# Kernel optimization log

Hardware: AMD Instinct MI355X
Metric: run time of the kernel (lower is better)

Reference implementation:

```python
import jax, jax.numpy as jnp
import numpy as np

ENC_DIM, DEC_DIM, ATT_DIM = 512, 512, 256
B, T = 64, 4096


def setup_inputs() -> dict:
    key = jax.random.key(0)
    ks = jax.random.split(key, 7)
    s_enc = 1.0 / np.sqrt(ENC_DIM)
    s_dec = 1.0 / np.sqrt(DEC_DIM)
    s_att = 1.0 / np.sqrt(ATT_DIM)
    return {
        "encoder_features": jax.random.normal(ks[0], (B, T, ENC_DIM), jnp.float32),
        "decoder_hidden": jax.random.normal(ks[1], (B, DEC_DIM), jnp.float32),
        # encoder_proj: Linear(encoder_dim, attention_dim) with bias
        "W_enc": jax.random.uniform(ks[2], (ENC_DIM, ATT_DIM), jnp.float32, -s_enc, s_enc),
        "b_enc": jax.random.uniform(ks[3], (ATT_DIM,), jnp.float32, -s_enc, s_enc),
        # decoder_proj: Linear(decoder_dim, attention_dim, bias=False)
        "W_dec": jax.random.uniform(ks[4], (DEC_DIM, ATT_DIM), jnp.float32, -s_dec, s_dec),
        # attention_vector: Linear(attention_dim, 1) with bias
        "v_att": jax.random.uniform(ks[5], (ATT_DIM,), jnp.float32, -s_att, s_att),
        "b_att": jax.random.uniform(ks[6], (), jnp.float32, -s_att, s_att),
    }


def reference(encoder_features, decoder_hidden, W_enc, b_enc, W_dec, v_att, b_att):
    # (B,T,A) = (B,T,E)@(E,A) + b
    enc_proj = jnp.einsum("bte,ea->bta", encoder_features, W_enc) + b_enc
    # (B,1,A)
    dec_proj = (decoder_hidden @ W_dec)[:, None, :]
    energy = jnp.tanh(enc_proj + dec_proj)                      # (B,T,A)
    scores = jnp.einsum("bta,a->bt", energy, v_att) + b_att     # (B,T)
    attention_weights = jax.nn.softmax(scores, axis=1)          # (B,T)
    context = jnp.einsum("bt,bte->be", attention_weights, encoder_features)
    return (context, attention_weights)
```

## Files before the change

kernel.cpp:

```cpp
#include <hip/hip_runtime.h>
#include <hip/hip_bf16.h>

#define E_DIM 512
#define D_DIM 512
#define A_DIM 256
#define B_SZ  64
#define T_SZ  4096
#define TT    64
#define NTB   (T_SZ / TT)
#define LDT   (E_DIM + 8)

typedef __bf16 bf16_t;
typedef bf16_t bf16x8 __attribute__((ext_vector_type(8)));
typedef float  f32x4  __attribute__((ext_vector_type(4)));

__device__ __forceinline__ unsigned short f2bf(float x) {
    union { float f; unsigned int u; } v; v.f = x;
    unsigned int u = v.u;
    return (unsigned short)((u + 0x7FFFu + ((u >> 16) & 1u)) >> 16);
}
__device__ __forceinline__ float bf_lo(unsigned int pk) {
    union { unsigned int u; float f; } v; v.u = pk << 16; return v.f;
}
__device__ __forceinline__ float bf_hi(unsigned int pk) {
    union { unsigned int u; float f; } v; v.u = pk & 0xFFFF0000u; return v.f;
}
__device__ __forceinline__ float tanh_fast(float x) {
    x = fminf(8.0f, fmaxf(-8.0f, x));
    float e = __expf(2.0f * x);
    return 1.0f - 2.0f * __builtin_amdgcn_rcpf(e + 1.0f);
}

__global__ __launch_bounds__(256) void prep_kernel(
    const float* __restrict__ dec, const float* __restrict__ W_enc,
    const float* __restrict__ b_enc, const float* __restrict__ W_dec,
    float* __restrict__ dp, unsigned short* __restrict__ Wt)
{
    const int bid = blockIdx.x, tid = threadIdx.x;
    if (bid < B_SZ) {
        float s = b_enc[tid];
        const float* dr = dec + bid * D_DIM;
        #pragma unroll 8
        for (int d = 0; d < D_DIM; ++d)
            s = fmaf(dr[d], W_dec[d * A_DIM + tid], s);
        dp[bid * A_DIM + tid] = s;
    } else {
        int base = (bid - B_SZ) * 2048;
        #pragma unroll
        for (int i = 0; i < 8; ++i) {
            int idx = base + tid + i * 256;
            int a = idx >> 9, e = idx & 511;
            Wt[idx] = f2bf(W_enc[e * A_DIM + a]);
        }
    }
}

__global__ __launch_bounds__(256, 2) void attn_main(
    const float* __restrict__ enc, const unsigned short* __restrict__ Wt,
    const float* __restrict__ dpg, const float* __restrict__ vatt,
    float* __restrict__ u_out, float* __restrict__ ctx_part)
{
    const int tb = blockIdx.x, b = blockIdx.y;
    const int tid = threadIdx.x;
    __shared__ unsigned short tile[TT * LDT];
    __shared__ float spart[4][TT];
    __shared__ float uu[TT];
    __shared__ float dp_s[A_DIM];
    __shared__ float vv[A_DIM];

    dp_s[tid] = dpg[b * A_DIM + tid];
    vv[tid]   = vatt[tid];

    const float4* src = (const float4*)(enc + ((size_t)b * T_SZ + (size_t)tb * TT) * E_DIM);
    #pragma unroll 4
    for (int it = 0; it < 32; ++it) {
        int idx = tid + it * 256;
        int r = idx >> 7, c = idx & 127;
        float4 v4 = src[idx];
        ushort4 h;
        h.x = f2bf(v4.x); h.y = f2bf(v4.y); h.z = f2bf(v4.z); h.w = f2bf(v4.w);
        *(ushort4*)&tile[r * LDT + c * 4] = h;
    }
    __syncthreads();

    const int w = tid >> 6, lane = tid & 63;
    const int m16 = lane & 15, q = lane >> 4;
    f32x4 acc[4][4];
    #pragma unroll
    for (int mi = 0; mi < 4; ++mi)
        #pragma unroll
        for (int ni = 0; ni < 4; ++ni)
            acc[mi][ni] = (f32x4){0.f, 0.f, 0.f, 0.f};

    for (int k0 = 0; k0 < E_DIM; k0 += 32) {
        const int ka = k0 + q * 8;
        bf16x8 afr[4], bfr[4];
        #pragma unroll
        for (int mi = 0; mi < 4; ++mi)
            afr[mi] = *(const bf16x8*)&tile[(mi * 16 + m16) * LDT + ka];
        #pragma unroll
        for (int ni = 0; ni < 4; ++ni)
            bfr[ni] = *(const bf16x8*)&Wt[(w * 64 + ni * 16 + m16) * E_DIM + ka];
        #pragma unroll
        for (int mi = 0; mi < 4; ++mi)
            #pragma unroll
            for (int ni = 0; ni < 4; ++ni)
                acc[mi][ni] = __builtin_amdgcn_mfma_f32_16x16x32_bf16(
                    afr[mi], bfr[ni], acc[mi][ni], 0, 0, 0);
    }

    float va[4], dpv[4];
    #pragma unroll
    for (int ni = 0; ni < 4; ++ni) {
        int a = w * 64 + ni * 16 + m16;
        va[ni] = vv[a]; dpv[ni] = dp_s[a];
    }
    #pragma unroll
    for (int mi = 0; mi < 4; ++mi) {
        #pragma unroll
        for (int r = 0; r < 4; ++r) {
            float p = 0.f;
            #pragma unroll
            for (int ni = 0; ni < 4; ++ni)
                p += va[ni] * tanh_fast(acc[mi][ni][r] + dpv[ni]);
            p += __shfl_xor(p, 1); p += __shfl_xor(p, 2);
            p += __shfl_xor(p, 4); p += __shfl_xor(p, 8);
            if (m16 == 0) spart[w][mi * 16 + q * 4 + r] = p;
        }
    }
    __syncthreads();

    if (tid < TT) {
        float s = spart[0][tid] + spart[1][tid] + spart[2][tid] + spart[3][tid];
        float e = __expf(s);
        uu[tid] = e;
        u_out[(size_t)b * T_SZ + (size_t)tb * TT + tid] = e;
    }
    __syncthreads();

    float c0 = 0.f, c1 = 0.f;
    #pragma unroll 4
    for (int t = 0; t < TT; ++t) {
        float ut = uu[t];
        unsigned int pk = *(const unsigned int*)&tile[t * LDT + 2 * tid];
        c0 = fmaf(ut, bf_lo(pk), c0);
        c1 = fmaf(ut, bf_hi(pk), c1);
    }
    float2 st; st.x = c0; st.y = c1;
    ((float2*)(ctx_part + ((size_t)tb * B_SZ + b) * E_DIM))[tid] = st;
}

__global__ __launch_bounds__(256) void finalize_kernel(
    const float* __restrict__ u, const float* __restrict__ ctx_part,
    float* __restrict__ out)
{
    const int b = blockIdx.x, tid = threadIdx.x;
    __shared__ float red[256];
    const float* ub = u + (size_t)b * T_SZ;
    float s = 0.f;
    for (int i = tid; i < T_SZ; i += 256) s += ub[i];
    red[tid] = s; __syncthreads();
    for (int st = 128; st > 0; st >>= 1) {
        if (tid < st) red[tid] += red[tid + st];
        __syncthreads();
    }
    const float invS = 1.0f / red[0];
    float* wout = out + B_SZ * E_DIM + (size_t)b * T_SZ;
    for (int i = tid; i < T_SZ; i += 256) wout[i] = ub[i] * invS;
    for (int e = tid; e < E_DIM; e += 256) {
        float c = 0.f;
        #pragma unroll 8
        for (int t = 0; t < NTB; ++t)
            c += ctx_part[((size_t)t * B_SZ + b) * E_DIM + e];
        out[(size_t)b * E_DIM + e] = c * invS;
    }
}

extern "C" void kernel_launch(void* const* d_in, const int* in_sizes, int n_in,
                              void* d_out, int out_size, void* d_ws, size_t ws_size,
                              hipStream_t stream) {
    const float* enc   = (const float*)d_in[0];
    const float* dec   = (const float*)d_in[1];
    const float* W_enc = (const float*)d_in[2];
    const float* b_enc = (const float*)d_in[3];
    const float* W_dec = (const float*)d_in[4];
    const float* v_att = (const float*)d_in[5];
    float* out = (float*)d_out;

    char* ws = (char*)d_ws;
    unsigned short* Wt = (unsigned short*)(ws);
    float* dp          = (float*)(ws + 262144);
    float* u           = (float*)(ws + 327680);
    float* ctx_part    = (float*)(ws + 1376256);

    prep_kernel<<<128, 256, 0, stream>>>(dec, W_enc, b_enc, W_dec, dp, Wt);
    attn_main<<<dim3(NTB, B_SZ), 256, 0, stream>>>(enc, Wt, dp, v_att, u, ctx_part);
    finalize_kernel<<<B_SZ, 256, 0, stream>>>(u, ctx_part, out);
}
```

Measured before the change: 849.2 us.

## Double attn_main block to 512 threads, splitting attention columns across eight waves

```diff
diff --git a/kernel.cpp b/kernel.cpp
--- a/kernel.cpp
+++ b/kernel.cpp
@@ -55,7 +55,7 @@
     }
 }
 
-__global__ __launch_bounds__(256, 2) void attn_main(
+__global__ __launch_bounds__(512, 4) void attn_main(
     const float* __restrict__ enc, const unsigned short* __restrict__ Wt,
     const float* __restrict__ dpg, const float* __restrict__ vatt,
     float* __restrict__ u_out, float* __restrict__ ctx_part)
@@ -63,18 +63,21 @@
     const int tb = blockIdx.x, b = blockIdx.y;
     const int tid = threadIdx.x;
     __shared__ unsigned short tile[TT * LDT];
-    __shared__ float spart[4][TT];
+    __shared__ float spart[8][TT];
     __shared__ float uu[TT];
     __shared__ float dp_s[A_DIM];
     __shared__ float vv[A_DIM];
-
-    dp_s[tid] = dpg[b * A_DIM + tid];
-    vv[tid]   = vatt[tid];
+    __shared__ float ctx_red[E_DIM];
+
+    if (tid < A_DIM) {
+        dp_s[tid] = dpg[b * A_DIM + tid];
+        vv[tid]   = vatt[tid];
+    }
 
     const float4* src = (const float4*)(enc + ((size_t)b * T_SZ + (size_t)tb * TT) * E_DIM);
     #pragma unroll 4
-    for (int it = 0; it < 32; ++it) {
-        int idx = tid + it * 256;
+    for (int it = 0; it < 16; ++it) {
+        int idx = tid + it * 512;
         int r = idx >> 7, c = idx & 127;
         float4 v4 = src[idx];
         ushort4 h;
@@ -85,44 +88,44 @@
 
     const int w = tid >> 6, lane = tid & 63;
     const int m16 = lane & 15, q = lane >> 4;
-    f32x4 acc[4][4];
+    f32x4 acc[4][2];
     #pragma unroll
     for (int mi = 0; mi < 4; ++mi)
         #pragma unroll
-        for (int ni = 0; ni < 4; ++ni)
+        for (int ni = 0; ni < 2; ++ni)
             acc[mi][ni] = (f32x4){0.f, 0.f, 0.f, 0.f};
 
+    const unsigned short* WtW = Wt + (size_t)(w * 32) * E_DIM;
+    #pragma unroll 2
     for (int k0 = 0; k0 < E_DIM; k0 += 32) {
         const int ka = k0 + q * 8;
-        bf16x8 afr[4], bfr[4];
+        bf16x8 afr[4], bfr[2];
+        #pragma unroll
+        for (int ni = 0; ni < 2; ++ni)
+            bfr[ni] = *(const bf16x8*)&WtW[(ni * 16 + m16) * E_DIM + ka];
         #pragma unroll
         for (int mi = 0; mi < 4; ++mi)
             afr[mi] = *(const bf16x8*)&tile[(mi * 16 + m16) * LDT + ka];
         #pragma unroll
-        for (int ni = 0; ni < 4; ++ni)
-            bfr[ni] = *(const bf16x8*)&Wt[(w * 64 + ni * 16 + m16) * E_DIM + ka];
-        #pragma unroll
         for (int mi = 0; mi < 4; ++mi)
             #pragma unroll
-            for (int ni = 0; ni < 4; ++ni)
+            for (int ni = 0; ni < 2; ++ni)
                 acc[mi][ni] = __builtin_amdgcn_mfma_f32_16x16x32_bf16(
                     afr[mi], bfr[ni], acc[mi][ni], 0, 0, 0);
     }
 
-    float va[4], dpv[4];
+    float va[2], dpv[2];
     #pragma unroll
-    for (int ni = 0; ni < 4; ++ni) {
-        int a = w * 64 + ni * 16 + m16;
+    for (int ni = 0; ni < 2; ++ni) {
+        int a = w * 32 + ni * 16 + m16;
         va[ni] = vv[a]; dpv[ni] = dp_s[a];
     }
     #pragma unroll
     for (int mi = 0; mi < 4; ++mi) {
         #pragma unroll
         for (int r = 0; r < 4; ++r) {
-            float p = 0.f;
-            #pragma unroll
-            for (int ni = 0; ni < 4; ++ni)
-                p += va[ni] * tanh_fast(acc[mi][ni][r] + dpv[ni]);
+            float p = va[0] * tanh_fast(acc[mi][0][r] + dpv[0])
+                    + va[1] * tanh_fast(acc[mi][1][r] + dpv[1]);
             p += __shfl_xor(p, 1); p += __shfl_xor(p, 2);
             p += __shfl_xor(p, 4); p += __shfl_xor(p, 8);
             if (m16 == 0) spart[w][mi * 16 + q * 4 + r] = p;
@@ -131,23 +134,35 @@
     __syncthreads();
 
     if (tid < TT) {
-        float s = spart[0][tid] + spart[1][tid] + spart[2][tid] + spart[3][tid];
+        float s = 0.f;
+        #pragma unroll
+        for (int w8 = 0; w8 < 8; ++w8) s += spart[w8][tid];
         float e = __expf(s);
         uu[tid] = e;
         u_out[(size_t)b * T_SZ + (size_t)tb * TT + tid] = e;
     }
     __syncthreads();
 
-    float c0 = 0.f, c1 = 0.f;
-    #pragma unroll 4
-    for (int t = 0; t < TT; ++t) {
-        float ut = uu[t];
-        unsigned int pk = *(const unsigned int*)&tile[t * LDT + 2 * tid];
-        c0 = fmaf(ut, bf_lo(pk), c0);
-        c1 = fmaf(ut, bf_hi(pk), c1);
-    }
-    float2 st; st.x = c0; st.y = c1;
-    ((float2*)(ctx_part + ((size_t)tb * B_SZ + b) * E_DIM))[tid] = st;
+    {
+        const int c2 = tid & 255, h = tid >> 8;
+        float c0 = 0.f, c1 = 0.f;
+        #pragma unroll 8
+        for (int i = 0; i < 32; ++i) {
+            int t = h * 32 + i;
+            float ut = uu[t];
+            unsigned int pk = *(const unsigned int*)&tile[t * LDT + 2 * c2];
+            c0 = fmaf(ut, bf_lo(pk), c0);
+            c1 = fmaf(ut, bf_hi(pk), c1);
+        }
+        if (h == 1) { ctx_red[2 * c2] = c0; ctx_red[2 * c2 + 1] = c1; }
+        __syncthreads();
+        if (h == 0) {
+            c0 += ctx_red[2 * c2];
+            c1 += ctx_red[2 * c2 + 1];
+            float2 st; st.x = c0; st.y = c1;
+            ((float2*)(ctx_part + ((size_t)tb * B_SZ + b) * E_DIM))[c2] = st;
+        }
+    }
 }
 
 __global__ __launch_bounds__(256) void finalize_kernel(
@@ -194,6 +209,6 @@
     float* ctx_part    = (float*)(ws + 1376256);
 
     prep_kernel<<<128, 256, 0, stream>>>(dec, W_enc, b_enc, W_dec, dp, Wt);
-    attn_main<<<dim3(NTB, B_SZ), 256, 0, stream>>>(enc, Wt, dp, v_att, u, ctx_part);
+    attn_main<<<dim3(NTB, B_SZ), 512, 0, stream>>>(enc, Wt, dp, v_att, u, ctx_part);
     finalize_kernel<<<B_SZ, 256, 0, stream>>>(u, ctx_part, out);
 }
```

After: 840.0 us. No clear change (-1.1%).
